# Performance work log

Measured on AMD Instinct MI355X. Metric: run time of the kernel, lower is better.

## Reference

```python
import jax, jax.numpy as jnp
import numpy as np

N_NODES = 100000
N_EDGES = 1600000
K_HOPS = 10


def setup_inputs() -> dict:
    key = jax.random.key(0)
    ks = jax.random.split(key, 8)
    x = jax.random.normal(ks[0], (N_NODES, 512), dtype=jnp.float32)
    edge_src = jax.random.randint(ks[1], (N_EDGES,), 0, N_NODES, dtype=jnp.int32)
    edge_dst = jax.random.randint(ks[2], (N_EDGES,), 0, N_NODES, dtype=jnp.int32)
    # positive, roughly degree-normalized edge weights (stand-in for sym-normalized adj)
    edge_weight = jax.random.uniform(ks[3], (N_EDGES,), dtype=jnp.float32) / 16.0
    node_index = jax.random.randint(ks[4], (10000,), 0, N_NODES, dtype=jnp.int32)
    W1 = jax.random.normal(ks[5], (512, 64), dtype=jnp.float32) * 0.05
    W2 = jax.random.normal(ks[6], (64, 64), dtype=jnp.float32) * 0.05
    w_prop = jax.random.normal(ks[7], (64, 1), dtype=jnp.float32) * 0.05
    return {"x": x, "edge_src": edge_src, "edge_dst": edge_dst,
            "edge_weight": edge_weight, "node_index": node_index,
            "W1": W1, "W2": W2, "w_prop": w_prop}


def reference(x, edge_src, edge_dst, edge_weight, node_index, W1, W2, w_prop):
    # MLP (dropout is identity at inference, use_bias=False)
    h = jax.nn.relu(x @ W1)          # [N, 64]
    h = jax.nn.relu(h @ W2)          # [N, C]

    # K-hop sparse propagation: h_{k+1} = A @ h_k via edge-list SpMM
    def spmm(v):
        return jax.ops.segment_sum(edge_weight[:, None] * v[edge_src],
                                   edge_dst, num_segments=N_NODES)

    props = [h]
    cur = h
    for _ in range(K_HOPS):
        cur = spmm(cur)
        props.append(cur)
    H = jnp.stack(props, axis=1)     # [N, K+1, C]

    # sigmoid-gated combination across hops (DAGNN)
    score = jax.nn.sigmoid(H @ w_prop)        # [N, K+1, 1]
    out = jnp.sum(score * H, axis=1)          # [N, C]

    # gather requested nodes
    return out[node_index]                    # [n_idx, C]
```

## Files before the change

### kernel.cpp

```cpp
#include <hip/hip_runtime.h>
#include <hip/hip_bf16.h>

#define C 64

__device__ __forceinline__ float b2f(unsigned short s) {
    return __uint_as_float(((unsigned int)s) << 16);
}
__device__ __forceinline__ unsigned short f2b(float f) {
    unsigned int u = __float_as_uint(f);
    u = (u + 0x7FFF + ((u >> 16) & 1)) >> 16;
    return (unsigned short)u;
}

__launch_bounds__(256)
__global__ void mlp_kernel(const float* __restrict__ x,
                           const float* __restrict__ W1,
                           const float* __restrict__ W2,
                           float* __restrict__ h0,
                           unsigned short* __restrict__ hb, int nN)
{
    __shared__ float smem[8704];
    float (*As)[68] = (float(*)[68])smem;
    float (*Bs)[68] = (float(*)[68])(smem + 4352);
    float (*Hs)[68] = (float(*)[68])smem;
    float (*Ws)[68] = (float(*)[68])(smem + 4352);

    const int t  = threadIdx.x;
    const int ty = t >> 4;
    const int tx = t & 15;
    const int row0 = blockIdx.x * 64;

    const int srow = t >> 4;
    const int slk  = (t & 15) * 4;

    float acc[4][4] = {};

    for (int k0 = 0; k0 < 512; k0 += 64) {
        #pragma unroll
        for (int h = 0; h < 4; ++h) {
            int r = srow + 16 * h;
            int grow = row0 + r;
            float4 v = make_float4(0.f, 0.f, 0.f, 0.f);
            if (grow < nN) v = *(const float4*)&x[(size_t)grow * 512 + k0 + slk];
            *(float4*)&As[r][slk] = v;
        }
        #pragma unroll
        for (int h = 0; h < 4; ++h) {
            int r = srow + 16 * h;
            *(float4*)&Bs[r][slk] = *(const float4*)&W1[(size_t)(k0 + r) * 64 + slk];
        }
        __syncthreads();

        for (int kk = 0; kk < 64; kk += 4) {
            float4 b0 = *(float4*)&Bs[kk + 0][tx * 4];
            float4 b1 = *(float4*)&Bs[kk + 1][tx * 4];
            float4 b2 = *(float4*)&Bs[kk + 2][tx * 4];
            float4 b3 = *(float4*)&Bs[kk + 3][tx * 4];
            #pragma unroll
            for (int i = 0; i < 4; ++i) {
                float4 a = *(float4*)&As[ty * 4 + i][kk];
                acc[i][0] += a.x * b0.x + a.y * b1.x + a.z * b2.x + a.w * b3.x;
                acc[i][1] += a.x * b0.y + a.y * b1.y + a.z * b2.y + a.w * b3.y;
                acc[i][2] += a.x * b0.z + a.y * b1.z + a.z * b2.z + a.w * b3.z;
                acc[i][3] += a.x * b0.w + a.y * b1.w + a.z * b2.w + a.w * b3.w;
            }
        }
        __syncthreads();
    }

    #pragma unroll
    for (int i = 0; i < 4; ++i) {
        float4 o;
        o.x = acc[i][0] > 0.f ? acc[i][0] : 0.f;
        o.y = acc[i][1] > 0.f ? acc[i][1] : 0.f;
        o.z = acc[i][2] > 0.f ? acc[i][2] : 0.f;
        o.w = acc[i][3] > 0.f ? acc[i][3] : 0.f;
        *(float4*)&Hs[ty * 4 + i][tx * 4] = o;
    }
    #pragma unroll
    for (int qq = 0; qq < 4; ++qq) {
        int r = srow + 16 * qq;
        *(float4*)&Ws[r][slk] = *(const float4*)&W2[(size_t)r * 64 + slk];
    }
    __syncthreads();

    float acc2[4][4] = {};
    for (int kk = 0; kk < 64; kk += 4) {
        float4 b0 = *(float4*)&Ws[kk + 0][tx * 4];
        float4 b1 = *(float4*)&Ws[kk + 1][tx * 4];
        float4 b2 = *(float4*)&Ws[kk + 2][tx * 4];
        float4 b3 = *(float4*)&Ws[kk + 3][tx * 4];
        #pragma unroll
        for (int i = 0; i < 4; ++i) {
            float4 a = *(float4*)&Hs[ty * 4 + i][kk];
            acc2[i][0] += a.x * b0.x + a.y * b1.x + a.z * b2.x + a.w * b3.x;
            acc2[i][1] += a.x * b0.y + a.y * b1.y + a.z * b2.y + a.w * b3.y;
            acc2[i][2] += a.x * b0.z + a.y * b1.z + a.z * b2.z + a.w * b3.z;
            acc2[i][3] += a.x * b0.w + a.y * b1.w + a.z * b2.w + a.w * b3.w;
        }
    }

    #pragma unroll
    for (int i = 0; i < 4; ++i) {
        int grow = row0 + ty * 4 + i;
        if (grow < nN) {
            float4 o;
            o.x = acc2[i][0] > 0.f ? acc2[i][0] : 0.f;
            o.y = acc2[i][1] > 0.f ? acc2[i][1] : 0.f;
            o.z = acc2[i][2] > 0.f ? acc2[i][2] : 0.f;
            o.w = acc2[i][3] > 0.f ? acc2[i][3] : 0.f;
            *(float4*)&h0[(size_t)grow * 64 + tx * 4] = o;
            ushort4 ob = make_ushort4(f2b(o.x), f2b(o.y), f2b(o.z), f2b(o.w));
            *(ushort4*)&hb[(size_t)grow * 64 + tx * 4] = ob;
        }
    }
}

__launch_bounds__(256)
__global__ void count_kernel(const int* __restrict__ dst, int* __restrict__ rowptr, int nE)
{
    int e = blockIdx.x * 256 + threadIdx.x;
    if (e < nE) atomicAdd(&rowptr[dst[e]], 1);
}

__launch_bounds__(256)
__global__ void scanA(int* __restrict__ deg, int* __restrict__ bsum, int nN)
{
    __shared__ int ts[256];
    const int t = threadIdx.x;
    const int base = blockIdx.x * 1024 + t * 4;
    int v0 = 0, v1 = 0, v2 = 0, v3 = 0;
    if (base + 3 < nN) {
        int4 v = *(const int4*)&deg[base];
        v0 = v.x; v1 = v.y; v2 = v.z; v3 = v.w;
    } else {
        if (base + 0 < nN) v0 = deg[base + 0];
        if (base + 1 < nN) v1 = deg[base + 1];
        if (base + 2 < nN) v2 = deg[base + 2];
        if (base + 3 < nN) v3 = deg[base + 3];
    }
    int s = v0 + v1 + v2 + v3;
    ts[t] = s;
    __syncthreads();
    for (int d = 1; d < 256; d <<= 1) {
        int xv = (t >= d) ? ts[t - d] : 0;
        __syncthreads();
        ts[t] += xv;
        __syncthreads();
    }
    if (t == 255) bsum[blockIdx.x] = ts[255];
    int e0 = ts[t] - s;
    int e1 = e0 + v0;
    int e2 = e1 + v1;
    int e3 = e2 + v2;
    if (base + 3 < nN) {
        *(int4*)&deg[base] = make_int4(e0, e1, e2, e3);
    } else {
        if (base + 0 < nN) deg[base + 0] = e0;
        if (base + 1 < nN) deg[base + 1] = e1;
        if (base + 2 < nN) deg[base + 2] = e2;
        if (base + 3 < nN) deg[base + 3] = e3;
    }
}

__launch_bounds__(256)
__global__ void scanB(int* __restrict__ bsum, int nB)
{
    __shared__ int ts[256];
    const int t = threadIdx.x;
    int v = (t < nB) ? bsum[t] : 0;
    ts[t] = v;
    __syncthreads();
    for (int d = 1; d < 256; d <<= 1) {
        int xv = (t >= d) ? ts[t - d] : 0;
        __syncthreads();
        ts[t] += xv;
        __syncthreads();
    }
    if (t < nB) bsum[t] = ts[t] - v;
}

__launch_bounds__(256)
__global__ void scanC(int* __restrict__ deg, const int* __restrict__ bsum, int nN)
{
    const int i4 = (blockIdx.x * 256 + threadIdx.x) * 4;
    if (i4 >= nN) return;
    const int b = bsum[i4 >> 10];
    if (i4 + 3 < nN) {
        int4 v = *(int4*)&deg[i4];
        v.x += b; v.y += b; v.z += b; v.w += b;
        *(int4*)&deg[i4] = v;
    } else {
        for (int j = 0; j < 4 && i4 + j < nN; ++j) deg[i4 + j] += b;
    }
}

__launch_bounds__(256)
__global__ void fill_kernel(const int* __restrict__ src, const int* __restrict__ dst,
                            const float* __restrict__ w,
                            int* __restrict__ rowptr,
                            int2* __restrict__ cwp, int nE)
{
    int e = blockIdx.x * 256 + threadIdx.x;
    if (e >= nE) return;
    int d = dst[e];
    int pos = atomicAdd(&rowptr[d], 1);
    cwp[pos] = make_int2(src[e], __float_as_int(w[e]));
}

__launch_bounds__(256)
__global__ void spmm_fused(const int* __restrict__ rowptr,
                           const int2* __restrict__ cwp,
                           const unsigned short* __restrict__ cur,
                           unsigned short* __restrict__ nxt,
                           const int* __restrict__ idx,
                           const float* __restrict__ wp,
                           float* __restrict__ out,
                           int nN, int nI, int nodeBlocks)
{
    const int bid  = blockIdx.x;
    const int wid  = threadIdx.x >> 6;
    const int lane = threadIdx.x & 63;
    const int g = lane >> 3;
    const int q = lane & 7;

    int node, oi = -1;
    if (bid < nodeBlocks) {
        node = bid * 4 + wid;
        if (node >= nN) return;
    } else {
        oi = (bid - nodeBlocks) * 4 + wid;
        if (oi >= nI) return;
        node = idx[oi];
    }

    const int beg = (node == 0) ? 0 : rowptr[node - 1];
    const int end = rowptr[node];

    float a0[8] = {}, a1[8] = {};

    for (int e0 = beg; e0 < end; e0 += 64) {
        int el = e0 + lane;
        int2 ce = make_int2(0, 0);
        if (el < end) ce = cwp[el];
        int rem = end - e0; if (rem > 64) rem = 64;

        for (int s0 = 0; s0 < rem; s0 += 16) {
            int s = s0 + g;
            int   c0 = __shfl(ce.x, s);
            float w0 = __int_as_float(__shfl(ce.y, s));
            int   c1 = __shfl(ce.x, s + 8);
            float w1 = __int_as_float(__shfl(ce.y, s + 8));
            int4 r0 = *(const int4*)&cur[(size_t)c0 * 64 + q * 8];
            int4 r1 = *(const int4*)&cur[(size_t)c1 * 64 + q * 8];
            a0[0] += w0 * __uint_as_float((unsigned)r0.x << 16);
            a0[1] += w0 * __uint_as_float((unsigned)r0.x & 0xFFFF0000u);
            a0[2] += w0 * __uint_as_float((unsigned)r0.y << 16);
            a0[3] += w0 * __uint_as_float((unsigned)r0.y & 0xFFFF0000u);
            a0[4] += w0 * __uint_as_float((unsigned)r0.z << 16);
            a0[5] += w0 * __uint_as_float((unsigned)r0.z & 0xFFFF0000u);
            a0[6] += w0 * __uint_as_float((unsigned)r0.w << 16);
            a0[7] += w0 * __uint_as_float((unsigned)r0.w & 0xFFFF0000u);
            a1[0] += w1 * __uint_as_float((unsigned)r1.x << 16);
            a1[1] += w1 * __uint_as_float((unsigned)r1.x & 0xFFFF0000u);
            a1[2] += w1 * __uint_as_float((unsigned)r1.y << 16);
            a1[3] += w1 * __uint_as_float((unsigned)r1.y & 0xFFFF0000u);
            a1[4] += w1 * __uint_as_float((unsigned)r1.z << 16);
            a1[5] += w1 * __uint_as_float((unsigned)r1.z & 0xFFFF0000u);
            a1[6] += w1 * __uint_as_float((unsigned)r1.w << 16);
            a1[7] += w1 * __uint_as_float((unsigned)r1.w & 0xFFFF0000u);
        }
    }
    #pragma unroll
    for (int j = 0; j < 8; ++j) a0[j] += a1[j];

    #pragma unroll
    for (int j = 0; j < 8; ++j) {
        a0[j] += __shfl_xor(a0[j], 8);
        a0[j] += __shfl_xor(a0[j], 16);
        a0[j] += __shfl_xor(a0[j], 32);
    }

    if (oi < 0) {
        if (g == 0) {
            int4 ob;
            ob.x = (int)(((unsigned)f2b(a0[1]) << 16) | (unsigned)f2b(a0[0]));
            ob.y = (int)(((unsigned)f2b(a0[3]) << 16) | (unsigned)f2b(a0[2]));
            ob.z = (int)(((unsigned)f2b(a0[5]) << 16) | (unsigned)f2b(a0[4]));
            ob.w = (int)(((unsigned)f2b(a0[7]) << 16) | (unsigned)f2b(a0[6]));
            *(int4*)&nxt[(size_t)node * 64 + q * 8] = ob;
        }
    } else {
        float s = 0.f;
        #pragma unroll
        for (int j = 0; j < 8; ++j) s += a0[j] * wp[q * 8 + j];
        s += __shfl_xor(s, 1); s += __shfl_xor(s, 2); s += __shfl_xor(s, 4);
        float gate = 1.f / (1.f + __expf(-s));
        if (g == 0) {
            float* op = &out[(size_t)oi * 64 + q * 8];
            float4 p0 = *(float4*)op;
            float4 p1 = *(float4*)(op + 4);
            p0.x += gate * a0[0]; p0.y += gate * a0[1];
            p0.z += gate * a0[2]; p0.w += gate * a0[3];
            p1.x += gate * a0[4]; p1.y += gate * a0[5];
            p1.z += gate * a0[6]; p1.w += gate * a0[7];
            *(float4*)op = p0;
            *(float4*)(op + 4) = p1;
        }
    }
}

__launch_bounds__(256)
__global__ void gate_gather(const float* __restrict__ h,
                            const int* __restrict__ idx,
                            const float* __restrict__ wp,
                            float* __restrict__ out, int nI)
{
    int gid = blockIdx.x * 256 + threadIdx.x;
    int i = gid >> 6;
    if (i >= nI) return;
    int c = gid & 63;
    int n = idx[i];
    float v = h[(size_t)n * 64 + c];
    float s = v * wp[c];
    #pragma unroll
    for (int off = 32; off > 0; off >>= 1)
        s += __shfl_xor(s, off);
    float gate = 1.f / (1.f + __expf(-s));
    out[gid] = gate * v;
}

extern "C" void kernel_launch(void* const* d_in, const int* in_sizes, int n_in,
                              void* d_out, int out_size, void* d_ws, size_t ws_size,
                              hipStream_t stream) {
    const float* x    = (const float*)d_in[0];
    const int*   esrc = (const int*)d_in[1];
    const int*   edst = (const int*)d_in[2];
    const float* ew   = (const float*)d_in[3];
    const int*   nidx = (const int*)d_in[4];
    const float* W1   = (const float*)d_in[5];
    const float* W2   = (const float*)d_in[6];
    const float* wp   = (const float*)d_in[7];
    float* out = (float*)d_out;

    const int nN = in_sizes[0] / 512;
    const int nE = in_sizes[1];
    const int nI = in_sizes[4];

    float*          h0     = (float*)d_ws;
    unsigned short* bufA   = (unsigned short*)(h0 + (size_t)nN * C);
    unsigned short* bufB   = bufA + (size_t)nN * C;
    int*            rowptr = (int*)(bufB + (size_t)nN * C);
    int2*           cwp    = (int2*)(rowptr + nN);
    int*            bsum   = (int*)bufB;

    const int nB = (nN + 1023) / 1024;

    hipMemsetAsync(rowptr, 0, (size_t)nN * sizeof(int), stream);
    count_kernel<<<(nE + 255) / 256, 256, 0, stream>>>(edst, rowptr, nE);
    scanA<<<nB, 256, 0, stream>>>(rowptr, bsum, nN);
    scanB<<<1, 256, 0, stream>>>(bsum, nB);
    scanC<<<nB, 256, 0, stream>>>(rowptr, bsum, nN);
    fill_kernel<<<(nE + 255) / 256, 256, 0, stream>>>(esrc, edst, ew, rowptr, cwp, nE);

    mlp_kernel<<<(nN + 63) / 64, 256, 0, stream>>>(x, W1, W2, h0, bufA, nN);

    gate_gather<<<(nI * 64 + 255) / 256, 256, 0, stream>>>(h0, nidx, wp, out, nI);

    unsigned short* cur = bufA;
    unsigned short* nxt = bufB;
    const int nodeBlocks = (nN + 3) / 4;
    const int idxBlocks  = (nI + 3) / 4;
    for (int k = 0; k < 10; ++k) {
        const int nb = (k == 9) ? 0 : nodeBlocks;
        spmm_fused<<<nb + idxBlocks, 256, 0, stream>>>(
            rowptr, cwp, cur, nxt, nidx, wp, out, nN, nI, nb);
        unsigned short* tmp = cur; cur = nxt; nxt = tmp;
    }
}
```

Measured before the change: 954.2 us.

## Partition CSR by source segment and run SpMM in four cache-blocked passes

Builds a CSR keyed by (source segment, destination), with four source ranges, so that each SpMM pass only gathers from about a quarter of the bf16 feature table and that slice can stay in cache. Each hop becomes four launches that accumulate partial sums in an fp32 buffer, reusing the h0 storage. The final pass converts the sum to bf16 and fuses the gated output for the indexed nodes. The last hop runs a dedicated index-only kernel. In exchange it adds repeated fp32 accumulator reads and writes, four times as many launches, and narrower 8-byte gathers per lane.

```diff
diff --git a/kernel.cpp b/kernel.cpp
--- a/kernel.cpp
+++ b/kernel.cpp
@@ -117,27 +117,28 @@
 }
 
 __launch_bounds__(256)
-__global__ void count_kernel(const int* __restrict__ dst, int* __restrict__ rowptr, int nE)
+__global__ void count4(const int* __restrict__ src, const int* __restrict__ dst,
+                       int* __restrict__ rp4, int nE, int nN, int segW)
 {
     int e = blockIdx.x * 256 + threadIdx.x;
-    if (e < nE) atomicAdd(&rowptr[dst[e]], 1);
-}
-
-__launch_bounds__(256)
-__global__ void scanA(int* __restrict__ deg, int* __restrict__ bsum, int nN)
+    if (e < nE) atomicAdd(&rp4[(src[e] / segW) * nN + dst[e]], 1);
+}
+
+__launch_bounds__(256)
+__global__ void scanA(int* __restrict__ deg, int* __restrict__ bsum, int L)
 {
     __shared__ int ts[256];
     const int t = threadIdx.x;
     const int base = blockIdx.x * 1024 + t * 4;
     int v0 = 0, v1 = 0, v2 = 0, v3 = 0;
-    if (base + 3 < nN) {
+    if (base + 3 < L) {
         int4 v = *(const int4*)&deg[base];
         v0 = v.x; v1 = v.y; v2 = v.z; v3 = v.w;
     } else {
-        if (base + 0 < nN) v0 = deg[base + 0];
-        if (base + 1 < nN) v1 = deg[base + 1];
-        if (base + 2 < nN) v2 = deg[base + 2];
-        if (base + 3 < nN) v3 = deg[base + 3];
+        if (base + 0 < L) v0 = deg[base + 0];
+        if (base + 1 < L) v1 = deg[base + 1];
+        if (base + 2 < L) v2 = deg[base + 2];
+        if (base + 3 < L) v3 = deg[base + 3];
     }
     int s = v0 + v1 + v2 + v3;
     ts[t] = s;
@@ -153,25 +154,25 @@
     int e1 = e0 + v0;
     int e2 = e1 + v1;
     int e3 = e2 + v2;
-    if (base + 3 < nN) {
+    if (base + 3 < L) {
         *(int4*)&deg[base] = make_int4(e0, e1, e2, e3);
     } else {
-        if (base + 0 < nN) deg[base + 0] = e0;
-        if (base + 1 < nN) deg[base + 1] = e1;
-        if (base + 2 < nN) deg[base + 2] = e2;
-        if (base + 3 < nN) deg[base + 3] = e3;
-    }
-}
-
-__launch_bounds__(256)
+        if (base + 0 < L) deg[base + 0] = e0;
+        if (base + 1 < L) deg[base + 1] = e1;
+        if (base + 2 < L) deg[base + 2] = e2;
+        if (base + 3 < L) deg[base + 3] = e3;
+    }
+}
+
+__launch_bounds__(512)
 __global__ void scanB(int* __restrict__ bsum, int nB)
 {
-    __shared__ int ts[256];
+    __shared__ int ts[512];
     const int t = threadIdx.x;
     int v = (t < nB) ? bsum[t] : 0;
     ts[t] = v;
     __syncthreads();
-    for (int d = 1; d < 256; d <<= 1) {
+    for (int d = 1; d < 512; d <<= 1) {
         int xv = (t >= d) ? ts[t - d] : 0;
         __syncthreads();
         ts[t] += xv;
@@ -181,132 +182,172 @@
 }
 
 __launch_bounds__(256)
-__global__ void scanC(int* __restrict__ deg, const int* __restrict__ bsum, int nN)
+__global__ void scanC(int* __restrict__ deg, const int* __restrict__ bsum, int L)
 {
     const int i4 = (blockIdx.x * 256 + threadIdx.x) * 4;
-    if (i4 >= nN) return;
+    if (i4 >= L) return;
     const int b = bsum[i4 >> 10];
-    if (i4 + 3 < nN) {
+    if (i4 + 3 < L) {
         int4 v = *(int4*)&deg[i4];
         v.x += b; v.y += b; v.z += b; v.w += b;
         *(int4*)&deg[i4] = v;
     } else {
-        for (int j = 0; j < 4 && i4 + j < nN; ++j) deg[i4 + j] += b;
-    }
-}
-
-__launch_bounds__(256)
-__global__ void fill_kernel(const int* __restrict__ src, const int* __restrict__ dst,
-                            const float* __restrict__ w,
-                            int* __restrict__ rowptr,
-                            int2* __restrict__ cwp, int nE)
+        for (int j = 0; j < 4 && i4 + j < L; ++j) deg[i4 + j] += b;
+    }
+}
+
+__launch_bounds__(256)
+__global__ void fill4(const int* __restrict__ src, const int* __restrict__ dst,
+                      const float* __restrict__ w,
+                      int* __restrict__ rp4,
+                      int2* __restrict__ cwp, int nE, int nN, int segW)
 {
     int e = blockIdx.x * 256 + threadIdx.x;
     if (e >= nE) return;
-    int d = dst[e];
-    int pos = atomicAdd(&rowptr[d], 1);
+    int pos = atomicAdd(&rp4[(src[e] / segW) * nN + dst[e]], 1);
     cwp[pos] = make_int2(src[e], __float_as_int(w[e]));
 }
 
 __launch_bounds__(256)
-__global__ void spmm_fused(const int* __restrict__ rowptr,
-                           const int2* __restrict__ cwp,
-                           const unsigned short* __restrict__ cur,
-                           unsigned short* __restrict__ nxt,
-                           const int* __restrict__ idx,
-                           const float* __restrict__ wp,
-                           float* __restrict__ out,
-                           int nN, int nI, int nodeBlocks)
+__global__ void spmm_seg(const int* __restrict__ rowptr4,
+                         const int2* __restrict__ cwp,
+                         const unsigned short* __restrict__ cur,
+                         float* __restrict__ acc,
+                         unsigned short* __restrict__ nxt,
+                         const int* __restrict__ idx,
+                         const float* __restrict__ wp,
+                         float* __restrict__ out,
+                         int nN, int nI, int seg, int mode, int nodeBlocks)
 {
     const int bid  = blockIdx.x;
     const int wid  = threadIdx.x >> 6;
     const int lane = threadIdx.x & 63;
-    const int g = lane >> 3;
-    const int q = lane & 7;
-
-    int node, oi = -1;
+    const int g = lane >> 4;
+    const int q = lane & 15;
+
     if (bid < nodeBlocks) {
-        node = bid * 4 + wid;
-        if (node >= nN) return;
+        const int n0 = (bid * 4 + wid) * 4;
+        for (int v = 0; v < 4; ++v) {
+            const int node = n0 + v;
+            if (node >= nN) return;
+            const int row = seg * nN + node;
+            const int beg = (row == 0) ? 0 : rowptr4[row - 1];
+            const int end = rowptr4[row];
+            float a0 = 0.f, a1 = 0.f, a2 = 0.f, a3 = 0.f;
+            for (int e = beg + g; e < end; e += 4) {
+                int2 ce = cwp[e];
+                float w = __int_as_float(ce.y);
+                ushort4 r = *(const ushort4*)&cur[(size_t)ce.x * 64 + q * 4];
+                a0 += w * b2f(r.x); a1 += w * b2f(r.y);
+                a2 += w * b2f(r.z); a3 += w * b2f(r.w);
+            }
+            a0 += __shfl_xor(a0, 16); a0 += __shfl_xor(a0, 32);
+            a1 += __shfl_xor(a1, 16); a1 += __shfl_xor(a1, 32);
+            a2 += __shfl_xor(a2, 16); a2 += __shfl_xor(a2, 32);
+            a3 += __shfl_xor(a3, 16); a3 += __shfl_xor(a3, 32);
+            if (g == 0) {
+                const size_t off = (size_t)node * 64 + q * 4;
+                if (mode == 0) {
+                    *(float4*)&acc[off] = make_float4(a0, a1, a2, a3);
+                } else {
+                    float4 p = *(float4*)&acc[off];
+                    p.x += a0; p.y += a1; p.z += a2; p.w += a3;
+                    if (mode == 1) {
+                        *(float4*)&acc[off] = p;
+                    } else {
+                        ushort4 ob = make_ushort4(f2b(p.x), f2b(p.y),
+                                                  f2b(p.z), f2b(p.w));
+                        *(ushort4*)&nxt[off] = ob;
+                    }
+                }
+            }
+        }
     } else {
-        oi = (bid - nodeBlocks) * 4 + wid;
+        const int oi = (bid - nodeBlocks) * 4 + wid;
         if (oi >= nI) return;
-        node = idx[oi];
-    }
-
-    const int beg = (node == 0) ? 0 : rowptr[node - 1];
-    const int end = rowptr[node];
-
-    float a0[8] = {}, a1[8] = {};
-
-    for (int e0 = beg; e0 < end; e0 += 64) {
-        int el = e0 + lane;
-        int2 ce = make_int2(0, 0);
-        if (el < end) ce = cwp[el];
-        int rem = end - e0; if (rem > 64) rem = 64;
-
-        for (int s0 = 0; s0 < rem; s0 += 16) {
-            int s = s0 + g;
-            int   c0 = __shfl(ce.x, s);
-            float w0 = __int_as_float(__shfl(ce.y, s));
-            int   c1 = __shfl(ce.x, s + 8);
-            float w1 = __int_as_float(__shfl(ce.y, s + 8));
-            int4 r0 = *(const int4*)&cur[(size_t)c0 * 64 + q * 8];
-            int4 r1 = *(const int4*)&cur[(size_t)c1 * 64 + q * 8];
-            a0[0] += w0 * __uint_as_float((unsigned)r0.x << 16);
-            a0[1] += w0 * __uint_as_float((unsigned)r0.x & 0xFFFF0000u);
-            a0[2] += w0 * __uint_as_float((unsigned)r0.y << 16);
-            a0[3] += w0 * __uint_as_float((unsigned)r0.y & 0xFFFF0000u);
-            a0[4] += w0 * __uint_as_float((unsigned)r0.z << 16);
-            a0[5] += w0 * __uint_as_float((unsigned)r0.z & 0xFFFF0000u);
-            a0[6] += w0 * __uint_as_float((unsigned)r0.w << 16);
-            a0[7] += w0 * __uint_as_float((unsigned)r0.w & 0xFFFF0000u);
-            a1[0] += w1 * __uint_as_float((unsigned)r1.x << 16);
-            a1[1] += w1 * __uint_as_float((unsigned)r1.x & 0xFFFF0000u);
-            a1[2] += w1 * __uint_as_float((unsigned)r1.y << 16);
-            a1[3] += w1 * __uint_as_float((unsigned)r1.y & 0xFFFF0000u);
-            a1[4] += w1 * __uint_as_float((unsigned)r1.z << 16);
-            a1[5] += w1 * __uint_as_float((unsigned)r1.z & 0xFFFF0000u);
-            a1[6] += w1 * __uint_as_float((unsigned)r1.w << 16);
-            a1[7] += w1 * __uint_as_float((unsigned)r1.w & 0xFFFF0000u);
-        }
-    }
-    #pragma unroll
-    for (int j = 0; j < 8; ++j) a0[j] += a1[j];
-
-    #pragma unroll
-    for (int j = 0; j < 8; ++j) {
-        a0[j] += __shfl_xor(a0[j], 8);
-        a0[j] += __shfl_xor(a0[j], 16);
-        a0[j] += __shfl_xor(a0[j], 32);
-    }
-
-    if (oi < 0) {
+        const int node = idx[oi];
+        const int row = seg * nN + node;
+        const int beg = (row == 0) ? 0 : rowptr4[row - 1];
+        const int end = rowptr4[row];
+        float a0 = 0.f, a1 = 0.f, a2 = 0.f, a3 = 0.f;
+        for (int e = beg + g; e < end; e += 4) {
+            int2 ce = cwp[e];
+            float w = __int_as_float(ce.y);
+            ushort4 r = *(const ushort4*)&cur[(size_t)ce.x * 64 + q * 4];
+            a0 += w * b2f(r.x); a1 += w * b2f(r.y);
+            a2 += w * b2f(r.z); a3 += w * b2f(r.w);
+        }
+        a0 += __shfl_xor(a0, 16); a0 += __shfl_xor(a0, 32);
+        a1 += __shfl_xor(a1, 16); a1 += __shfl_xor(a1, 32);
+        a2 += __shfl_xor(a2, 16); a2 += __shfl_xor(a2, 32);
+        a3 += __shfl_xor(a3, 16); a3 += __shfl_xor(a3, 32);
+        float4 p = make_float4(0.f, 0.f, 0.f, 0.f);
+        float s = 0.f;
         if (g == 0) {
-            int4 ob;
-            ob.x = (int)(((unsigned)f2b(a0[1]) << 16) | (unsigned)f2b(a0[0]));
-            ob.y = (int)(((unsigned)f2b(a0[3]) << 16) | (unsigned)f2b(a0[2]));
-            ob.z = (int)(((unsigned)f2b(a0[5]) << 16) | (unsigned)f2b(a0[4]));
-            ob.w = (int)(((unsigned)f2b(a0[7]) << 16) | (unsigned)f2b(a0[6]));
-            *(int4*)&nxt[(size_t)node * 64 + q * 8] = ob;
-        }
-    } else {
-        float s = 0.f;
-        #pragma unroll
-        for (int j = 0; j < 8; ++j) s += a0[j] * wp[q * 8 + j];
-        s += __shfl_xor(s, 1); s += __shfl_xor(s, 2); s += __shfl_xor(s, 4);
+            p = *(const float4*)&acc[(size_t)node * 64 + q * 4];
+            p.x += a0; p.y += a1; p.z += a2; p.w += a3;
+            s = p.x * wp[q * 4] + p.y * wp[q * 4 + 1]
+              + p.z * wp[q * 4 + 2] + p.w * wp[q * 4 + 3];
+        }
+        s += __shfl_xor(s, 1); s += __shfl_xor(s, 2);
+        s += __shfl_xor(s, 4); s += __shfl_xor(s, 8);
         float gate = 1.f / (1.f + __expf(-s));
         if (g == 0) {
-            float* op = &out[(size_t)oi * 64 + q * 8];
-            float4 p0 = *(float4*)op;
-            float4 p1 = *(float4*)(op + 4);
-            p0.x += gate * a0[0]; p0.y += gate * a0[1];
-            p0.z += gate * a0[2]; p0.w += gate * a0[3];
-            p1.x += gate * a0[4]; p1.y += gate * a0[5];
-            p1.z += gate * a0[6]; p1.w += gate * a0[7];
-            *(float4*)op = p0;
-            *(float4*)(op + 4) = p1;
-        }
+            float* op = &out[(size_t)oi * 64 + q * 4];
+            float4 pr = *(float4*)op;
+            pr.x += gate * p.x; pr.y += gate * p.y;
+            pr.z += gate * p.z; pr.w += gate * p.w;
+            *(float4*)op = pr;
+        }
+    }
+}
+
+__launch_bounds__(256)
+__global__ void spmm_idx(const int* __restrict__ rowptr4,
+                         const int2* __restrict__ cwp,
+                         const unsigned short* __restrict__ cur,
+                         const int* __restrict__ idx,
+                         const float* __restrict__ wp,
+                         float* __restrict__ out,
+                         int nN, int nI)
+{
+    const int oi = blockIdx.x * 4 + (threadIdx.x >> 6);
+    if (oi >= nI) return;
+    const int lane = threadIdx.x & 63;
+    const int g = lane >> 4;
+    const int q = lane & 15;
+    const int node = idx[oi];
+
+    float a0 = 0.f, a1 = 0.f, a2 = 0.f, a3 = 0.f;
+    for (int s4 = 0; s4 < 4; ++s4) {
+        const int row = s4 * nN + node;
+        const int beg = (row == 0) ? 0 : rowptr4[row - 1];
+        const int end = rowptr4[row];
+        for (int e = beg + g; e < end; e += 4) {
+            int2 ce = cwp[e];
+            float w = __int_as_float(ce.y);
+            ushort4 r = *(const ushort4*)&cur[(size_t)ce.x * 64 + q * 4];
+            a0 += w * b2f(r.x); a1 += w * b2f(r.y);
+            a2 += w * b2f(r.z); a3 += w * b2f(r.w);
+        }
+    }
+    a0 += __shfl_xor(a0, 16); a0 += __shfl_xor(a0, 32);
+    a1 += __shfl_xor(a1, 16); a1 += __shfl_xor(a1, 32);
+    a2 += __shfl_xor(a2, 16); a2 += __shfl_xor(a2, 32);
+    a3 += __shfl_xor(a3, 16); a3 += __shfl_xor(a3, 32);
+    float s = 0.f;
+    if (g == 0)
+        s = a0 * wp[q * 4] + a1 * wp[q * 4 + 1]
+          + a2 * wp[q * 4 + 2] + a3 * wp[q * 4 + 3];
+    s += __shfl_xor(s, 1); s += __shfl_xor(s, 2);
+    s += __shfl_xor(s, 4); s += __shfl_xor(s, 8);
+    float gate = 1.f / (1.f + __expf(-s));
+    if (g == 0) {
+        float* op = &out[(size_t)oi * 64 + q * 4];
+        float4 pr = *(float4*)op;
+        pr.x += gate * a0; pr.y += gate * a1;
+        pr.z += gate * a2; pr.w += gate * a3;
+        *(float4*)op = pr;
     }
 }
 
@@ -350,18 +391,20 @@
     float*          h0     = (float*)d_ws;
     unsigned short* bufA   = (unsigned short*)(h0 + (size_t)nN * C);
     unsigned short* bufB   = bufA + (size_t)nN * C;
-    int*            rowptr = (int*)(bufB + (size_t)nN * C);
-    int2*           cwp    = (int2*)(rowptr + nN);
+    int*            rp4    = (int*)(bufB + (size_t)nN * C);
+    int2*           cwp    = (int2*)(rp4 + (size_t)4 * nN);
     int*            bsum   = (int*)bufB;
 
-    const int nB = (nN + 1023) / 1024;
-
-    hipMemsetAsync(rowptr, 0, (size_t)nN * sizeof(int), stream);
-    count_kernel<<<(nE + 255) / 256, 256, 0, stream>>>(edst, rowptr, nE);
-    scanA<<<nB, 256, 0, stream>>>(rowptr, bsum, nN);
-    scanB<<<1, 256, 0, stream>>>(bsum, nB);
-    scanC<<<nB, 256, 0, stream>>>(rowptr, bsum, nN);
-    fill_kernel<<<(nE + 255) / 256, 256, 0, stream>>>(esrc, edst, ew, rowptr, cwp, nE);
+    const int segW = (nN + 3) / 4;
+    const int L    = 4 * nN;
+    const int nB   = (L + 1023) / 1024;
+
+    hipMemsetAsync(rp4, 0, (size_t)L * sizeof(int), stream);
+    count4<<<(nE + 255) / 256, 256, 0, stream>>>(esrc, edst, rp4, nE, nN, segW);
+    scanA<<<nB, 256, 0, stream>>>(rp4, bsum, L);
+    scanB<<<1, 512, 0, stream>>>(bsum, nB);
+    scanC<<<nB, 256, 0, stream>>>(rp4, bsum, L);
+    fill4<<<(nE + 255) / 256, 256, 0, stream>>>(esrc, edst, ew, rp4, cwp, nE, nN, segW);
 
     mlp_kernel<<<(nN + 63) / 64, 256, 0, stream>>>(x, W1, W2, h0, bufA, nN);
 
@@ -369,12 +412,16 @@
 
     unsigned short* cur = bufA;
     unsigned short* nxt = bufB;
-    const int nodeBlocks = (nN + 3) / 4;
+    const int nodeBlocks = (nN + 15) / 16;
     const int idxBlocks  = (nI + 3) / 4;
-    for (int k = 0; k < 10; ++k) {
-        const int nb = (k == 9) ? 0 : nodeBlocks;
-        spmm_fused<<<nb + idxBlocks, 256, 0, stream>>>(
-            rowptr, cwp, cur, nxt, nidx, wp, out, nN, nI, nb);
+    for (int k = 0; k < 9; ++k) {
+        for (int s4 = 0; s4 < 4; ++s4) {
+            const int mode = (s4 == 0) ? 0 : ((s4 == 3) ? 2 : 1);
+            const int grid = nodeBlocks + ((s4 == 3) ? idxBlocks : 0);
+            spmm_seg<<<grid, 256, 0, stream>>>(
+                rp4, cwp, cur, h0, nxt, nidx, wp, out, nN, nI, s4, mode, nodeBlocks);
+        }
         unsigned short* tmp = cur; cur = nxt; nxt = tmp;
     }
-}
+    spmm_idx<<<idxBlocks, 256, 0, stream>>>(rp4, cwp, cur, nidx, wp, out, nN, nI);
+}
```

Result: slower. 1.614 ms (+69.1%).
